# Performance work log

Measured on AMD Instinct MI355X. Metric: run time of the kernel, lower is better.

The kernel has to match this reference:

```python
import jax, jax.numpy as jnp
import numpy as np

WH, WW = 8, 8          # window size
DIM = 384
HEADS = 12
N = WH * WW            # tokens per window = 64


def _relative_position_index():
    ch, cw = np.meshgrid(np.arange(WH), np.arange(WW), indexing='ij')
    coords = np.stack([ch, cw]).reshape(2, -1)            # (2, N)
    rel = coords[:, :, None] - coords[:, None, :]         # (2, N, N)
    rel = rel.transpose(1, 2, 0).astype(np.int32)         # (N, N, 2)
    rel[:, :, 0] += WH - 1
    rel[:, :, 1] += WW - 1
    rel[:, :, 0] *= 2 * WW - 1
    return jnp.asarray(rel.sum(-1))                       # (N, N) int32


def setup_inputs() -> dict:
    key = jax.random.key(0)
    ks = jax.random.split(key, 6)
    B_ = 4096
    x = jax.random.normal(ks[0], (B_, N, DIM), dtype=jnp.float32)
    mask = jnp.zeros((B_, N, N), dtype=jnp.float32)       # nW == B_ here (B=1)
    qkv_w = jax.random.normal(ks[1], (DIM, 3 * DIM), dtype=jnp.float32) * 0.02
    qkv_b = jnp.zeros((3 * DIM,), dtype=jnp.float32)
    rpb_table = jax.random.normal(ks[2], ((2 * WH - 1) * (2 * WW - 1), HEADS), dtype=jnp.float32) * 0.02
    proj_w = jax.random.normal(ks[3], (DIM, DIM), dtype=jnp.float32) * 0.02
    proj_b = jnp.zeros((DIM,), dtype=jnp.float32)
    rpi = _relative_position_index()
    return {"x": x, "mask": mask, "qkv_w": qkv_w, "qkv_b": qkv_b,
            "rpb_table": rpb_table, "proj_w": proj_w, "proj_b": proj_b, "rpi": rpi}


def reference(x, mask, qkv_w, qkv_b, rpb_table, proj_w, proj_b, rpi):
    B_, n, C = x.shape
    hd = C // HEADS
    scale = hd ** -0.5
    qkv = (x @ qkv_w + qkv_b).reshape(B_, n, 3, HEADS, hd)
    q, k, v = qkv[:, :, 0], qkv[:, :, 1], qkv[:, :, 2]    # (B_, n, H, hd)
    attn = jnp.einsum('bnhd,bmhd->bhnm', q * scale, k)    # (B_, H, n, n)
    bias = rpb_table[rpi]                                 # (n, n, H)
    attn = attn + jnp.transpose(bias, (2, 0, 1))[None]    # add rel-pos bias
    nW = mask.shape[0]
    attn = attn.reshape(B_ // nW, nW, HEADS, n, n) + mask[None, :, None]
    attn = attn.reshape(B_, HEADS, n, n)
    attn = jax.nn.softmax(attn, axis=-1)
    out = jnp.einsum('bhnm,bmhd->bnhd', attn, v).reshape(B_, n, C)
    return out @ proj_w + proj_b
```

## Files before the change

kernel.cpp:

```cpp
#include <hip/hip_runtime.h>
#include <hip/hip_bf16.h>

typedef unsigned short u16;
typedef unsigned int   u32;
typedef __attribute__((ext_vector_type(8))) __bf16 bf16x8;
typedef __attribute__((ext_vector_type(4))) float  f32x4;

#define NWIN   4096
#define SEQ    64
#define DIMC   384
#define NHEAD  12
#define HDIM   32
#define NROWS  262144
#define NQKV   1152

__device__ __forceinline__ u16 f2bf(float f){
  u32 x = __float_as_uint(f);
  return (u16)((x + 0x7fffu + ((x >> 16) & 1u)) >> 16);
}

__device__ __forceinline__ void gload_lds16(const u16* g, u16* l){
  __builtin_amdgcn_global_load_lds(
      (const __attribute__((address_space(1))) void*)g,
      (__attribute__((address_space(3))) void*)l, 16, 0, 0);
}

__device__ __forceinline__ f32x4 mfma_bf16(bf16x8 a, bf16x8 b, f32x4 c){
  return __builtin_amdgcn_mfma_f32_16x16x32_bf16(a, b, c, 0, 0, 0);
}

__global__ void prep_x(const float* __restrict__ x, u16* __restrict__ xb){
  size_t i = ((size_t)blockIdx.x * 256 + threadIdx.x) * 8;
  f32x4 a = *(const f32x4*)(x + i);
  f32x4 b = *(const f32x4*)(x + i + 4);
  union { u16 u[8]; bf16x8 v; } o;
  #pragma unroll
  for(int j=0;j<4;j++) o.u[j]   = f2bf(a[j]);
  #pragma unroll
  for(int j=0;j<4;j++) o.u[4+j] = f2bf(b[j]);
  *(bf16x8*)(xb + i) = o.v;
}

__global__ void prep_w(const float* __restrict__ qw, const float* __restrict__ pw,
                       const float* __restrict__ rpb, const int* __restrict__ rpi,
                       u16* __restrict__ wqT, u16* __restrict__ wpT,
                       float* __restrict__ biasT){
  int id = blockIdx.x * 256 + threadIdx.x;
  if (id < NQKV*DIMC){
    int n = id / DIMC, k = id % DIMC;
    wqT[id] = f2bf(qw[(size_t)k*NQKV + n]);
  } else if (id < NQKV*DIMC + DIMC*DIMC){
    int j = id - NQKV*DIMC;
    int n = j / DIMC, k = j % DIMC;
    wpT[j] = f2bf(pw[(size_t)k*DIMC + n]);
  } else {
    int j = id - (NQKV*DIMC + DIMC*DIMC);
    int h = j / 4096, nm = j % 4096;
    biasT[j] = rpb[rpi[nm]*NHEAD + h];
  }
}

template<int NB, int EPI>
__global__ __launch_bounds__(256, 2) void gemm_bt(
    const u16* __restrict__ A, const u16* __restrict__ Bt,
    const float* __restrict__ bias,
    u16* __restrict__ oq, u16* __restrict__ okk, u16* __restrict__ ov,
    float* __restrict__ of)
{
  __shared__ u16 Al[2][8192];
  __shared__ u16 Bl[2][8192];
  const int bid0 = blockIdx.x;
  const int bid = (bid0 & 7) * ((2048*NB) >> 3) + (bid0 >> 3);
  const int bm = bid / NB, bn = bid % NB;
  const size_t m0 = (size_t)bm * 128;
  const int n0 = bn * 128;
  const int tid = threadIdx.x, wv = tid >> 6, ln = tid & 63;
  const int wr = wv >> 1, wc = wv & 1;
  const int cl = ln & 15, q8 = ln >> 4;

  f32x4 acc[4][4];
  const f32x4 zero4 = {0.f,0.f,0.f,0.f};
  #pragma unroll
  for(int i=0;i<4;i++)
    #pragma unroll
    for(int j=0;j<4;j++) acc[i][j] = zero4;

  auto stage = [&](int bufi, int kt){
    #pragma unroll
    for(int c=0;c<4;c++){
      int un  = (wv*4+c)*64 + ln;
      int row = un >> 3;
      int u   = (un & 7) ^ (row & 7);
      gload_lds16(A  + (m0 + row)*DIMC + kt*64 + u*8, &Al[bufi][(wv*4+c)*512]);
      gload_lds16(Bt + (size_t)(n0 + row)*DIMC + kt*64 + u*8, &Bl[bufi][(wv*4+c)*512]);
    }
  };

  stage(0, 0);
  #pragma unroll
  for(int kt=0;kt<6;kt++){
    const int bufi = kt & 1;
    __syncthreads();
    if (kt < 5) stage(bufi^1, kt+1);
    #pragma unroll
    for(int ks=0;ks<2;ks++){
      bf16x8 af[4], bfr[4];
      #pragma unroll
      for(int i=0;i<4;i++){
        int row = wr*64 + i*16 + cl;
        int u = (ks*4 + q8) ^ (row & 7);
        af[i] = *(const bf16x8*)&Al[bufi][row*64 + u*8];
      }
      #pragma unroll
      for(int j=0;j<4;j++){
        int row = wc*64 + j*16 + cl;
        int u = (ks*4 + q8) ^ (row & 7);
        bfr[j] = *(const bf16x8*)&Bl[bufi][row*64 + u*8];
      }
      #pragma unroll
      for(int i=0;i<4;i++)
        #pragma unroll
        for(int j=0;j<4;j++)
          acc[i][j] = mfma_bf16(af[i], bfr[j], acc[i][j]);
    }
  }

  float bj[4];
  #pragma unroll
  for(int j=0;j<4;j++) bj[j] = bias[n0 + wc*64 + j*16 + cl];

  if (EPI == 0){
    const int t = n0 / DIMC;
    const int lc0 = n0 - t*DIMC + wc*64 + cl;
    u16* dst = (t==0) ? oq : (t==1) ? okk : ov;
    #pragma unroll
    for(int i=0;i<4;i++){
      size_t r0 = m0 + wr*64 + i*16 + q8*4;
      #pragma unroll
      for(int j=0;j<4;j++)
        #pragma unroll
        for(int r=0;r<4;r++)
          dst[(r0 + r)*DIMC + lc0 + j*16] = f2bf(acc[i][j][r] + bj[j]);
    }
  } else {
    const int lc0 = n0 + wc*64 + cl;
    #pragma unroll
    for(int i=0;i<4;i++){
      size_t r0 = m0 + wr*64 + i*16 + q8*4;
      #pragma unroll
      for(int j=0;j<4;j++)
        #pragma unroll
        for(int r=0;r<4;r++)
          of[(r0 + r)*DIMC + lc0 + j*16] = acc[i][j][r] + bj[j];
    }
  }
}

__global__ __launch_bounds__(256, 1) void qkv_attn(
    const u16* __restrict__ Xb, const u16* __restrict__ Wq,
    const float* __restrict__ qkvb, const float* __restrict__ biasT,
    const float* __restrict__ mask, u16* __restrict__ AO)
{
  __shared__ u16 xa[64*384];
  __shared__ u16 wl[4][2][2048];
  __shared__ u16 qk[4][4096];
  __shared__ u16 vt[4][2048];

  const int bid = blockIdx.x;
  const int L = (bid & 7) * ((NWIN*3) >> 3) + (bid >> 3);
  const int w = L / 3, hg = L % 3;
  const int tid = threadIdx.x, wv = tid >> 6, ln = tid & 63;
  const int cl = ln & 15, g = ln >> 4;
  const size_t rb = (size_t)w * SEQ;
  const int h = hg*4 + wv;
  const f32x4 zero4 = {0.f,0.f,0.f,0.f};
  const float scale = 0.17677669529663687f;

  float bb[3][2];
  #pragma unroll
  for(int p=0;p<3;p++)
    #pragma unroll
    for(int j=0;j<2;j++) bb[p][j] = qkvb[p*384 + h*32 + j*16 + cl];

  #pragma unroll
  for(int c=0;c<12;c++){
    int un = c*256 + tid;
    int row = un / 48, up = un % 48;
    int u = (up & 0x38) | ((up ^ row) & 7);
    gload_lds16(Xb + (rb + row)*DIMC + u*8, &xa[(c*256 + wv*64)*8]);
  }
  __syncthreads();

  auto stageW = [&](int s, int b){
    const int p = s/6, kt = s - p*6;
    const size_t nb = (size_t)(p*384 + h*32);
    #pragma unroll
    for(int c=0;c<4;c++){
      int un = c*64 + ln;
      int row = un >> 3;
      int u = (un & 7) ^ (row & 7);
      gload_lds16(Wq + (nb + row)*DIMC + kt*64 + u*8, &wl[wv][b][c*512]);
    }
  };

  f32x4 acc[4][2];
  stageW(0, 0);
  #pragma unroll
  for(int s=0;s<18;s++){
    if ((s % 6) == 0){
      #pragma unroll
      for(int i=0;i<4;i++){ acc[i][0] = zero4; acc[i][1] = zero4; }
    }
    if (s < 17){
      asm volatile("s_waitcnt lgkmcnt(0)" ::: "memory");
      __builtin_amdgcn_sched_barrier(0);
      stageW(s+1, (s+1)&1);
      asm volatile("s_waitcnt vmcnt(4)" ::: "memory");
    } else {
      asm volatile("s_waitcnt vmcnt(0)" ::: "memory");
    }
    __builtin_amdgcn_sched_barrier(0);
    const int kt = s % 6, b = s & 1;
    #pragma unroll
    for(int ks=0;ks<2;ks++){
      bf16x8 af[4], bw[2];
      #pragma unroll
      for(int i=0;i<4;i++){
        int row = i*16 + cl;
        int ug = kt*8 + ks*4 + g;
        int pu = (ug & 0x38) | ((ug ^ row) & 7);
        af[i] = *(const bf16x8*)&xa[row*384 + pu*8];
      }
      #pragma unroll
      for(int j=0;j<2;j++){
        int row = j*16 + cl;
        int u = (ks*4 + g) ^ (row & 7);
        bw[j] = *(const bf16x8*)&wl[wv][b][row*64 + u*8];
      }
      #pragma unroll
      for(int i=0;i<4;i++)
        #pragma unroll
        for(int j=0;j<2;j++)
          acc[i][j] = mfma_bf16(af[i], bw[j], acc[i][j]);
    }
    if (s == 5){
      #pragma unroll
      for(int i=0;i<4;i++)
        #pragma unroll
        for(int j=0;j<2;j++)
          #pragma unroll
          for(int r=0;r<4;r++){
            int tok = i*16 + g*4 + r;
            qk[wv][tok*32 + j*16 + cl] = f2bf((acc[i][j][r] + bb[0][j]) * scale);
          }
    }
    if (s == 11){
      #pragma unroll
      for(int i=0;i<4;i++)
        #pragma unroll
        for(int j=0;j<2;j++)
          #pragma unroll
          for(int r=0;r<4;r++){
            int tok = i*16 + g*4 + r;
            qk[wv][2048 + tok*32 + j*16 + cl] = f2bf(acc[i][j][r] + bb[1][j]);
          }
    }
    if (s == 17){
      #pragma unroll
      for(int i=0;i<4;i++)
        #pragma unroll
        for(int j=0;j<2;j++)
          #pragma unroll
          for(int r=0;r<4;r++){
            int tok = i*16 + g*4 + r, dh = j*16 + cl;
            vt[wv][dh*64 + (((tok>>3) ^ (dh&7))*8) + (tok&7)] =
                f2bf(acc[i][j][r] + bb[2][j]);
          }
    }
  }

  u16* ph = qk[wv];
  const u16* pv = vt[wv];

  bf16x8 aq[4], bk[4];
  #pragma unroll
  for(int i=0;i<4;i++) aq[i] = *(const bf16x8*)&ph[(i*16 + cl)*32 + g*8];
  #pragma unroll
  for(int j=0;j<4;j++) bk[j] = *(const bf16x8*)&ph[2048 + (j*16 + cl)*32 + g*8];
  f32x4 S[4][4];
  #pragma unroll
  for(int i=0;i<4;i++)
    #pragma unroll
    for(int j=0;j<4;j++)
      S[i][j] = mfma_bf16(aq[i], bk[j], zero4);

  float l[4][4];
  #pragma unroll
  for(int i=0;i<4;i++){
    #pragma unroll
    for(int r=0;r<4;r++){
      int row = i*16 + g*4 + r;
      float v0[4];
      #pragma unroll
      for(int j=0;j<4;j++){
        int col2 = j*16 + cl;
        v0[j] = S[i][j][r] + biasT[h*4096 + row*64 + col2]
                           + mask[(size_t)w*4096 + row*64 + col2];
      }
      float mx = fmaxf(fmaxf(v0[0],v0[1]), fmaxf(v0[2],v0[3]));
      #pragma unroll
      for(int s=1;s<16;s<<=1) mx = fmaxf(mx, __shfl_xor(mx, s));
      float sm = 0.f;
      #pragma unroll
      for(int j=0;j<4;j++){ v0[j] = __expf(v0[j]-mx); sm += v0[j]; }
      #pragma unroll
      for(int s=1;s<16;s<<=1) sm += __shfl_xor(sm, s);
      l[i][r] = sm;
      #pragma unroll
      for(int j=0;j<4;j++){
        int col2 = j*16 + cl;
        ph[row*64 + (((col2>>3) ^ (row&7))*8) + (col2&7)] = f2bf(v0[j]);
      }
    }
  }
  f32x4 O[4][2];
  #pragma unroll
  for(int i=0;i<4;i++){ O[i][0] = zero4; O[i][1] = zero4; }
  #pragma unroll
  for(int ks=0;ks<2;ks++){
    bf16x8 ap[4], bv[2];
    #pragma unroll
    for(int i=0;i<4;i++){
      int m = i*16 + cl;
      ap[i] = *(const bf16x8*)&ph[m*64 + (((ks*4+g) ^ (m&7))*8)];
    }
    #pragma unroll
    for(int j=0;j<2;j++){
      int n = j*16 + cl;
      bv[j] = *(const bf16x8*)&pv[n*64 + (((ks*4+g) ^ (n&7))*8)];
    }
    #pragma unroll
    for(int i=0;i<4;i++)
      #pragma unroll
      for(int j=0;j<2;j++)
        O[i][j] = mfma_bf16(ap[i], bv[j], O[i][j]);
  }
  #pragma unroll
  for(int i=0;i<4;i++){
    #pragma unroll
    for(int r=0;r<4;r++){
      float inv = 1.0f / l[i][r];
      size_t orow = (rb + i*16 + g*4 + r)*DIMC + h*HDIM;
      AO[orow + cl]      = f2bf(O[i][0][r]*inv);
      AO[orow + 16 + cl] = f2bf(O[i][1][r]*inv);
    }
  }
}

extern "C" void kernel_launch(void* const* d_in, const int* in_sizes, int n_in,
                              void* d_out, int out_size, void* d_ws, size_t ws_size,
                              hipStream_t stream) {
  const float* x      = (const float*)d_in[0];
  const float* mask   = (const float*)d_in[1];
  const float* qkv_w  = (const float*)d_in[2];
  const float* qkv_b  = (const float*)d_in[3];
  const float* rpb    = (const float*)d_in[4];
  const float* proj_w = (const float*)d_in[5];
  const float* proj_b = (const float*)d_in[6];
  const int*   rpi    = (const int*)d_in[7];

  u16* xb  = (u16*)d_ws;
  u16* ao  = xb + (size_t)NROWS*DIMC;
  u16* wqT = ao + (size_t)NROWS*DIMC;
  u16* wpT = wqT + (size_t)NQKV*DIMC;
  float* biasT = (float*)(wpT + (size_t)DIMC*DIMC);

  prep_x<<<(NROWS*(size_t)DIMC)/(256*8), 256, 0, stream>>>(x, xb);
  prep_w<<<(NQKV*DIMC + DIMC*DIMC + NHEAD*4096)/256, 256, 0, stream>>>(
      qkv_w, proj_w, rpb, rpi, wqT, wpT, biasT);
  qkv_attn<<<NWIN*3, 256, 0, stream>>>(xb, wqT, qkv_b, biasT, mask, ao);
  gemm_bt<3,1><<<2048*3, 256, 0, stream>>>(ao, wpT, proj_b, nullptr, nullptr, nullptr,
                                           (float*)d_out);
}
```

Before: 1.608 ms.

## Load QKV GEMM operands directly from global memory, dropping LDS staging

Removes the shared-memory staging of the 64x384 X tile and the double-buffered per-wave weight tiles. MFMA operands are now read straight from global memory into registers. The launch bound rises from 1 to 3 blocks per SM. This cuts LDS use from about 80KB to 48KB so more blocks can be resident and latency can be hidden. The cost is that each wave now re-reads the X tile from global/L2 (four waves read the same X) and the explicit software prefetch pipeline is gone.

```diff
diff --git a/kernel.cpp b/kernel.cpp
--- a/kernel.cpp
+++ b/kernel.cpp
@@ -156,13 +156,11 @@
   }
 }
 
-__global__ __launch_bounds__(256, 1) void qkv_attn(
+__global__ __launch_bounds__(256, 3) void qkv_attn(
     const u16* __restrict__ Xb, const u16* __restrict__ Wq,
     const float* __restrict__ qkvb, const float* __restrict__ biasT,
     const float* __restrict__ mask, u16* __restrict__ AO)
 {
-  __shared__ u16 xa[64*384];
-  __shared__ u16 wl[4][2][2048];
   __shared__ u16 qk[4][4096];
   __shared__ u16 vt[4][2048];
 
@@ -182,68 +180,36 @@
     #pragma unroll
     for(int j=0;j<2;j++) bb[p][j] = qkvb[p*384 + h*32 + j*16 + cl];
 
-  #pragma unroll
-  for(int c=0;c<12;c++){
-    int un = c*256 + tid;
-    int row = un / 48, up = un % 48;
-    int u = (up & 0x38) | ((up ^ row) & 7);
-    gload_lds16(Xb + (rb + row)*DIMC + u*8, &xa[(c*256 + wv*64)*8]);
-  }
-  __syncthreads();
-
-  auto stageW = [&](int s, int b){
-    const int p = s/6, kt = s - p*6;
-    const size_t nb = (size_t)(p*384 + h*32);
-    #pragma unroll
-    for(int c=0;c<4;c++){
-      int un = c*64 + ln;
-      int row = un >> 3;
-      int u = (un & 7) ^ (row & 7);
-      gload_lds16(Wq + (nb + row)*DIMC + kt*64 + u*8, &wl[wv][b][c*512]);
-    }
-  };
-
-  f32x4 acc[4][2];
-  stageW(0, 0);
-  #pragma unroll
-  for(int s=0;s<18;s++){
-    if ((s % 6) == 0){
-      #pragma unroll
-      for(int i=0;i<4;i++){ acc[i][0] = zero4; acc[i][1] = zero4; }
-    }
-    if (s < 17){
-      asm volatile("s_waitcnt lgkmcnt(0)" ::: "memory");
-      __builtin_amdgcn_sched_barrier(0);
-      stageW(s+1, (s+1)&1);
-      asm volatile("s_waitcnt vmcnt(4)" ::: "memory");
-    } else {
-      asm volatile("s_waitcnt vmcnt(0)" ::: "memory");
-    }
-    __builtin_amdgcn_sched_barrier(0);
-    const int kt = s % 6, b = s & 1;
-    #pragma unroll
-    for(int ks=0;ks<2;ks++){
-      bf16x8 af[4], bw[2];
-      #pragma unroll
-      for(int i=0;i<4;i++){
-        int row = i*16 + cl;
-        int ug = kt*8 + ks*4 + g;
-        int pu = (ug & 0x38) | ((ug ^ row) & 7);
-        af[i] = *(const bf16x8*)&xa[row*384 + pu*8];
-      }
-      #pragma unroll
-      for(int j=0;j<2;j++){
-        int row = j*16 + cl;
-        int u = (ks*4 + g) ^ (row & 7);
-        bw[j] = *(const bf16x8*)&wl[wv][b][row*64 + u*8];
-      }
-      #pragma unroll
-      for(int i=0;i<4;i++)
-        #pragma unroll
-        for(int j=0;j<2;j++)
-          acc[i][j] = mfma_bf16(af[i], bw[j], acc[i][j]);
-    }
-    if (s == 5){
+  const u16* xrow[4];
+  #pragma unroll
+  for(int i=0;i<4;i++) xrow[i] = Xb + (rb + i*16 + cl)*DIMC + g*8;
+
+  #pragma unroll
+  for(int p=0;p<3;p++){
+    const u16* Wp = Wq + (size_t)(p*384 + h*32)*DIMC;
+    const u16* wrow0 = Wp + (size_t)(cl     )*DIMC + g*8;
+    const u16* wrow1 = Wp + (size_t)(cl + 16)*DIMC + g*8;
+    f32x4 acc[4][2];
+    #pragma unroll
+    for(int i=0;i<4;i++){ acc[i][0] = zero4; acc[i][1] = zero4; }
+    #pragma unroll
+    for(int kt=0;kt<6;kt++){
+      #pragma unroll
+      for(int ks=0;ks<2;ks++){
+        const int k0 = kt*64 + ks*32;
+        bf16x8 af[4], bw[2];
+        #pragma unroll
+        for(int i=0;i<4;i++) af[i] = *(const bf16x8*)(xrow[i] + k0);
+        bw[0] = *(const bf16x8*)(wrow0 + k0);
+        bw[1] = *(const bf16x8*)(wrow1 + k0);
+        #pragma unroll
+        for(int i=0;i<4;i++)
+          #pragma unroll
+          for(int j=0;j<2;j++)
+            acc[i][j] = mfma_bf16(af[i], bw[j], acc[i][j]);
+      }
+    }
+    if (p == 0){
       #pragma unroll
       for(int i=0;i<4;i++)
         #pragma unroll
@@ -253,8 +219,7 @@
             int tok = i*16 + g*4 + r;
             qk[wv][tok*32 + j*16 + cl] = f2bf((acc[i][j][r] + bb[0][j]) * scale);
           }
-    }
-    if (s == 11){
+    } else if (p == 1){
       #pragma unroll
       for(int i=0;i<4;i++)
         #pragma unroll
@@ -264,8 +229,7 @@
             int tok = i*16 + g*4 + r;
             qk[wv][2048 + tok*32 + j*16 + cl] = f2bf(acc[i][j][r] + bb[1][j]);
           }
-    }
-    if (s == 17){
+    } else {
       #pragma unroll
       for(int i=0;i<4;i++)
         #pragma unroll
```

New measurement: 2.236 ms. 39.1% more time.
